# Kernel optimization log

Measured on AMD Instinct MI355X. Metric: run time of the kernel, lower is better.

Reference implementation:

```python
import jax, jax.numpy as jnp
import numpy as np

# LDPC-like Tanner graph: N variable nodes, M check nodes, dv edges per variable
N_VAR = 8192
N_CHK = 4096
DV = 3
N_EDGE = N_VAR * DV  # 24576 = code.H.E
BATCH = 128
T = 30               # opt.T iterations
EPS = 1e-7


def setup_inputs() -> dict:
    key = jax.random.key(0)
    k1, k2 = jax.random.split(key)
    # channel LLRs for a batch of received codewords, shape (N_VAR, BATCH)
    chn_llr = jax.random.normal(k1, (N_VAR, BATCH), dtype=jnp.float32) * 2.0
    # Tanner graph edge lists: edge e connects variable edge_var[e] <-> check edge_chk[e]
    edge_var = jnp.repeat(jnp.arange(N_VAR, dtype=jnp.int32), DV)
    edge_chk = jax.random.randint(k2, (N_EDGE,), 0, N_CHK, dtype=jnp.int32)
    # gamma_logit = 0  ->  sigmoid = 0.5 = damping_init
    gamma_logit = jnp.zeros((1,), dtype=jnp.float32)
    return {"chn_llr": chn_llr, "gamma_logit": gamma_logit,
            "edge_var": edge_var, "edge_chk": edge_chk}


def reference(chn_llr, gamma_logit, edge_var, edge_chk):
    """T damped sum-product BP iterations over the Tanner graph.

    Returns stacked per-iteration posterior LLRs, shape (T, N_VAR, BATCH).
    """
    gamma = jax.nn.sigmoid(gamma_logit[0])  # damping gate, shared (tie=True)
    segsum = jax.ops.segment_sum

    def step(carry, _):
        msg_C2V, msg_V2C = carry  # each (N_EDGE, BATCH)
        # ---- variable -> check update (extrinsic sum), damped by gamma ----
        var_sum = segsum(msg_C2V, edge_var, num_segments=N_VAR)        # (N_VAR, B)
        v2c_new = chn_llr[edge_var] + var_sum[edge_var] - msg_C2V       # (E, B)
        msg_V2C = gamma * v2c_new + (1.0 - gamma) * msg_V2C
        # ---- check -> variable update (tanh product rule, log/sign domain) ----
        t = jnp.tanh(jnp.clip(msg_V2C, -15.0, 15.0) * 0.5)              # (E, B)
        logabs = jnp.log(jnp.maximum(jnp.abs(t), EPS))
        neg = (t < 0.0).astype(msg_V2C.dtype)
        chk_log = segsum(logabs, edge_chk, num_segments=N_CHK)          # (N_CHK, B)
        chk_neg = segsum(neg, edge_chk, num_segments=N_CHK)
        ext_log = chk_log[edge_chk] - logabs                            # exclude self
        ext_sign = 1.0 - 2.0 * jnp.mod(chk_neg[edge_chk] - neg, 2.0)
        prod = jnp.clip(ext_sign * jnp.exp(ext_log), -1.0 + EPS, 1.0 - EPS)
        msg_C2V = 2.0 * jnp.arctanh(prod)
        # ---- per-iteration posterior LLR output ----
        out = chn_llr + segsum(msg_C2V, edge_var, num_segments=N_VAR)   # (N_VAR, B)
        return (msg_C2V, msg_V2C), out

    init = (jnp.zeros((N_EDGE, BATCH), dtype=chn_llr.dtype),
            jnp.zeros((N_EDGE, BATCH), dtype=chn_llr.dtype))
    _, outputs = jax.lax.scan(step, init, None, length=T)
    return outputs  # (T, N_VAR, BATCH)
```

## Files before the change

### kernel.cpp

```cpp
#include <hip/hip_runtime.h>
#include <math.h>

#define N_VAR 8192
#define N_CHK 4096
#define DV 3
#define N_EDGE (N_VAR * DV)
#define BATCH 128
#define T_ITERS 30
#define ELLW 24
#define CHNK 8

#define LOG2E 1.44269504088896340736f
#define LN2   0.69314718055994530942f

__device__ __forceinline__ float tanh_half(float x) {
    float ex = __builtin_amdgcn_exp2f(x * LOG2E);
    float t = 1.0f - 2.0f * __builtin_amdgcn_rcpf(ex + 1.0f);
    float s = (x < 0.0f) ? -1.0f : 1.0f;
    return s * fmaxf(fabsf(t), 1e-7f);
}

__device__ __forceinline__ float atanh2(float p) {
    const float lim = 1.0f - 1e-7f;
    p = fminf(fmaxf(p, -lim), lim);
    return (__builtin_amdgcn_logf(1.0f + p) -
            __builtin_amdgcn_logf(1.0f - p)) * LN2;
}


__global__ void k_ell_scatter(const int* __restrict__ edge_chk,
                              int* __restrict__ deg_arr, int* __restrict__ ell_e) {
    int e = blockIdx.x * blockDim.x + threadIdx.x;
    if (e < N_EDGE) {
        int c = edge_chk[e];
        int pos = atomicAdd(&deg_arr[c], 1);
        if (pos < ELLW) ell_e[c * ELLW + pos] = e;
    }
}

__global__ __launch_bounds__(1024) void k_scan(const int* __restrict__ counts,
                                               int* __restrict__ ptr) {
    __shared__ int bufA[1024];
    __shared__ int bufB[1024];
    int t = threadIdx.x;
    int c0 = counts[4 * t + 0];
    int c1 = counts[4 * t + 1];
    int c2 = counts[4 * t + 2];
    int c3 = counts[4 * t + 3];
    int s = c0 + c1 + c2 + c3;
    bufA[t] = s;
    __syncthreads();
    int* src = bufA;
    int* dst = bufB;
    for (int off = 1; off < 1024; off *= 2) {
        int v = src[t];
        if (t >= off) v += src[t - off];
        dst[t] = v;
        __syncthreads();
        int* tmp = src; src = dst; dst = tmp;
    }
    int incl = src[t];
    int excl = incl - s;
    ptr[4 * t + 0] = excl;
    ptr[4 * t + 1] = excl + c0;
    ptr[4 * t + 2] = excl + c0 + c1;
    ptr[4 * t + 3] = excl + c0 + c1 + c2;
    if (t == 1023) ptr[N_CHK] = incl;
}

__global__ void k_slotmap(const int* __restrict__ ell_e,
                          const int* __restrict__ deg_arr,
                          const int* __restrict__ ptr,
                          int* __restrict__ slot_e) {
    int gid = blockIdx.x * 256 + threadIdx.x;
    if (gid < N_CHK * ELLW) {
        int c = gid / ELLW;
        int j = gid - c * ELLW;
        int d = deg_arr[c]; if (d > ELLW) d = ELLW;
        if (j < d) slot_e[ell_e[gid]] = ptr[c] + j;
    }
}

__global__ void k_pack(const int* __restrict__ slot_e, int4* __restrict__ recs) {
    int e = blockIdx.x * 256 + threadIdx.x;
    if (e < N_EDGE) {
        int v = e / 3;
        int4 r;
        r.x = slot_e[3 * v + 0];
        r.y = slot_e[3 * v + 1];
        r.z = slot_e[3 * v + 2];
        r.w = (v << 2) | (e - 3 * v);
        recs[slot_e[e]] = r;
    }
}


__global__ __launch_bounds__(128) void k_iter(
        const float* __restrict__ chn,
        const _Float16* __restrict__ c2v_prev,
        _Float16* __restrict__ c2v_curr,
        _Float16* __restrict__ v2c,
        float* __restrict__ out_prev,
        const int have_out,
        const float* __restrict__ gamma_logit,
        const int4* __restrict__ recs,
        const int* __restrict__ deg_arr,
        const int* __restrict__ ptr) {
    int c = blockIdx.x;
    int b = threadIdx.x;
    int deg = deg_arr[c];
    if (deg > ELLW) deg = ELLW;
    if (deg == 0) return;
    int base = ptr[c];
    float g = 1.0f / (1.0f + __builtin_amdgcn_exp2f(-gamma_logit[0] * LOG2E));
    float om = 1.0f - g;

    float tv[ELLW];

#define BATCH_BODY(J0)                                                         \
    {                                                                          \
        int4 r[CHNK]; float m0[CHNK], m1[CHNK], m2[CHNK], cv[CHNK], vo[CHNK];  \
        _Pragma("unroll")                                                      \
        for (int u = 0; u < CHNK; ++u) {                                       \
            int s = base + (J0) + u;                                           \
            s = (s < N_EDGE) ? s : (N_EDGE - 1);                               \
            r[u] = recs[s];                                                    \
        }                                                                      \
        _Pragma("unroll")                                                      \
        for (int u = 0; u < CHNK; ++u) {                                       \
            int s = base + (J0) + u;                                           \
            s = (s < N_EDGE) ? s : (N_EDGE - 1);                               \
            m0[u] = (float)c2v_prev[r[u].x * BATCH + b];                       \
            m1[u] = (float)c2v_prev[r[u].y * BATCH + b];                       \
            m2[u] = (float)c2v_prev[r[u].z * BATCH + b];                       \
            cv[u] = chn[(r[u].w >> 2) * BATCH + b];                            \
            vo[u] = (float)v2c[s * BATCH + b];                                 \
        }                                                                      \
        _Pragma("unroll")                                                      \
        for (int u = 0; u < CHNK; ++u) {                                       \
            int j = (J0) + u;                                                  \
            if (j < deg) {                                                     \
                int self = base + j;                                           \
                int v = r[u].w >> 2;                                           \
                float post = cv[u] + m0[u] + m1[u] + m2[u];                    \
                float cp = (r[u].x == self) ? m0[u]                            \
                           : ((r[u].y == self) ? m1[u] : m2[u]);               \
                float vn = g * (post - cp) + om * vo[u];                       \
                v2c[self * BATCH + b] = (_Float16)vn;                          \
                if (have_out && ((r[u].w & 3) == 0)) {                         \
                    __builtin_nontemporal_store(post,                          \
                        &out_prev[v * BATCH + b]);                             \
                }                                                              \
                float x = fminf(fmaxf(vn, -15.0f), 15.0f);                     \
                tv[j] = tanh_half(x);                                          \
            }                                                                  \
        }                                                                      \
    }

    BATCH_BODY(0)
    if (deg > CHNK) BATCH_BODY(CHNK)
    if (deg > 2 * CHNK) BATCH_BODY(2 * CHNK)
#undef BATCH_BODY

    float ext[ELLW];
    float run = 1.0f;
#pragma unroll
    for (int j = ELLW - 1; j >= 0; --j) {
        if (j < deg) { ext[j] = run; run *= tv[j]; }
    }
    float pfx = 1.0f;
#pragma unroll
    for (int j = 0; j < ELLW; ++j) {
        if (j < deg) {
            float p = pfx * ext[j];
            pfx *= tv[j];
            float m = atanh2(p);
            c2v_curr[(base + j) * BATCH + b] = (_Float16)m;
        }
    }
}


__global__ __launch_bounds__(256) void k_final(
        const float* __restrict__ chn, const _Float16* __restrict__ c2v,
        const int* __restrict__ slot_e, float* __restrict__ out_last) {
    int gid = blockIdx.x * 256 + threadIdx.x;
    int v = gid >> 7;
    int b = gid & 127;
    int s0 = slot_e[3 * v + 0];
    int s1 = slot_e[3 * v + 1];
    int s2 = slot_e[3 * v + 2];
    float acc = chn[gid] + (float)c2v[s0 * BATCH + b] +
                (float)c2v[s1 * BATCH + b] + (float)c2v[s2 * BATCH + b];
    __builtin_nontemporal_store(acc, &out_last[gid]);
}


extern "C" void kernel_launch(void* const* d_in, const int* in_sizes, int n_in,
                              void* d_out, int out_size, void* d_ws, size_t ws_size,
                              hipStream_t stream) {
    const float* chn         = (const float*)d_in[0];
    const float* gamma_logit = (const float*)d_in[1];
    const int* edge_chk      = (const int*)d_in[3];
    float* out = (float*)d_out;

    const size_t MSG = (size_t)N_EDGE * BATCH;
    _Float16* c2vA   = (_Float16*)d_ws;
    _Float16* c2vB   = c2vA + MSG;
    _Float16* v2c    = c2vB + MSG;
    int4* recs       = (int4*)(v2c + MSG);
    int* slot_e      = (int*)(recs + N_EDGE);
    int* ell_e       = slot_e + N_EDGE;
    int* deg_arr     = ell_e + (size_t)N_CHK * ELLW;
    int* ptr         = deg_arr + N_CHK;

    (void)hipMemsetAsync(c2vA, 0, MSG * sizeof(_Float16), stream);
    (void)hipMemsetAsync(v2c, 0, MSG * sizeof(_Float16), stream);
    (void)hipMemsetAsync(slot_e, 0, (size_t)N_EDGE * sizeof(int), stream);
    (void)hipMemsetAsync(deg_arr, 0, N_CHK * sizeof(int), stream);

    k_ell_scatter<<<(N_EDGE + 255) / 256, 256, 0, stream>>>(edge_chk, deg_arr,
                                                            ell_e);
    k_scan<<<1, 1024, 0, stream>>>(deg_arr, ptr);
    k_slotmap<<<(N_CHK * ELLW + 255) / 256, 256, 0, stream>>>(ell_e, deg_arr,
                                                              ptr, slot_e);
    k_pack<<<(N_EDGE + 255) / 256, 256, 0, stream>>>(slot_e, recs);

    const size_t SLICE = (size_t)N_VAR * BATCH;
    _Float16* bufs[2] = {c2vA, c2vB};
    for (int t = 0; t < T_ITERS; ++t) {
        const _Float16* prev = bufs[t & 1];
        _Float16* curr = bufs[(t + 1) & 1];
        float* out_prev = (t == 0) ? out : out + (size_t)(t - 1) * SLICE;
        k_iter<<<N_CHK, 128, 0, stream>>>(chn, prev, curr, v2c, out_prev,
                                          (t > 0) ? 1 : 0, gamma_logit, recs,
                                          deg_arr, ptr);
    }
    k_final<<<(N_VAR * BATCH) / 256, 256, 0, stream>>>(
        chn, bufs[T_ITERS & 1], slot_e, out + (size_t)(T_ITERS - 1) * SLICE);
}
```

Measured before the change: 618.2 us.

## Split fused check kernel into variable-node and check-node kernels with half2 packing

Replaces the single per-check kernel with two launches per iteration. A variable-node kernel computes posteriors once per variable, updates the damped V2C messages in variable order and writes clipped values into a check-slot-ordered array. A check-node kernel then only gathers those values and runs the tanh/atanh product rule. Both kernels process two batch lanes per thread using half2/float2 vectors. This avoids each check edge re-gathering three C2V messages plus the channel value, at the cost of an extra kernel launch per iteration and an additional intermediate array round trip through memory.

```diff
diff --git a/kernel.cpp b/kernel.cpp
--- a/kernel.cpp
+++ b/kernel.cpp
@@ -6,12 +6,16 @@
 #define DV 3
 #define N_EDGE (N_VAR * DV)
 #define BATCH 128
+#define HB (BATCH / 2)
 #define T_ITERS 30
 #define ELLW 24
 #define CHNK 8
 
 #define LOG2E 1.44269504088896340736f
 #define LN2   0.69314718055994530942f
+
+typedef _Float16 h2 __attribute__((ext_vector_type(2)));
+typedef float f2 __attribute__((ext_vector_type(2)));
 
 __device__ __forceinline__ float tanh_half(float x) {
     float ex = __builtin_amdgcn_exp2f(x * LOG2E);
@@ -81,118 +85,146 @@
     }
 }
 
-__global__ void k_pack(const int* __restrict__ slot_e, int4* __restrict__ recs) {
-    int e = blockIdx.x * 256 + threadIdx.x;
-    if (e < N_EDGE) {
-        int v = e / 3;
-        int4 r;
-        r.x = slot_e[3 * v + 0];
-        r.y = slot_e[3 * v + 1];
-        r.z = slot_e[3 * v + 2];
-        r.w = (v << 2) | (e - 3 * v);
-        recs[slot_e[e]] = r;
-    }
-}
-
-
-__global__ __launch_bounds__(128) void k_iter(
+__global__ void k_slot4(const int* __restrict__ slot_e, int4* __restrict__ slot4) {
+    int v = blockIdx.x * 256 + threadIdx.x;
+    if (v < N_VAR) {
+        int4 s;
+        s.x = slot_e[3 * v + 0];
+        s.y = slot_e[3 * v + 1];
+        s.z = slot_e[3 * v + 2];
+        s.w = 0;
+        slot4[v] = s;
+    }
+}
+
+
+__global__ __launch_bounds__(256) void k_var(
         const float* __restrict__ chn,
-        const _Float16* __restrict__ c2v_prev,
-        _Float16* __restrict__ c2v_curr,
-        _Float16* __restrict__ v2c,
+        const h2* __restrict__ c2v_prev,
+        h2* __restrict__ v2c,
+        h2* __restrict__ x_arr,
         float* __restrict__ out_prev,
         const int have_out,
         const float* __restrict__ gamma_logit,
-        const int4* __restrict__ recs,
+        const int4* __restrict__ slot4) {
+    int gid = blockIdx.x * 256 + threadIdx.x;
+    int v = gid >> 6;
+    int bb = gid & 63;
+    float g = 1.0f / (1.0f + __builtin_amdgcn_exp2f(-gamma_logit[0] * LOG2E));
+    float om = 1.0f - g;
+
+    int4 s4 = slot4[v];
+    int sl[3] = {s4.x, s4.y, s4.z};
+    h2 c0 = c2v_prev[s4.x * HB + bb];
+    h2 c1 = c2v_prev[s4.y * HB + bb];
+    h2 c2 = c2v_prev[s4.z * HB + bb];
+    f2 ch = ((const f2*)chn)[v * HB + bb];
+
+    float p0 = ch.x + (float)c0.x + (float)c1.x + (float)c2.x;
+    float p1 = ch.y + (float)c0.y + (float)c1.y + (float)c2.y;
+    if (have_out) {
+        f2 o; o.x = p0; o.y = p1;
+        __builtin_nontemporal_store(o, &((f2*)out_prev)[v * HB + bb]);
+    }
+
+    float cc0[3] = {(float)c0.x, (float)c1.x, (float)c2.x};
+    float cc1[3] = {(float)c0.y, (float)c1.y, (float)c2.y};
+#pragma unroll
+    for (int i = 0; i < 3; ++i) {
+        int vi = i * (N_VAR * HB) + v * HB + bb;
+        h2 vo = v2c[vi];
+        float vn0 = g * (p0 - cc0[i]) + om * (float)vo.x;
+        float vn1 = g * (p1 - cc1[i]) + om * (float)vo.y;
+        h2 w; w.x = (_Float16)vn0; w.y = (_Float16)vn1;
+        v2c[vi] = w;
+        float x0 = fminf(fmaxf(vn0, -15.0f), 15.0f);
+        float x1 = fminf(fmaxf(vn1, -15.0f), 15.0f);
+        h2 xw; xw.x = (_Float16)x0; xw.y = (_Float16)x1;
+        x_arr[sl[i] * HB + bb] = xw;
+    }
+}
+
+
+__global__ __launch_bounds__(256) void k_chk(
+        const h2* __restrict__ x_arr,
+        h2* __restrict__ c2v_curr,
         const int* __restrict__ deg_arr,
         const int* __restrict__ ptr) {
-    int c = blockIdx.x;
-    int b = threadIdx.x;
+    int c = blockIdx.x * 4 + (threadIdx.x >> 6);
+    int bb = threadIdx.x & 63;
     int deg = deg_arr[c];
     if (deg > ELLW) deg = ELLW;
     if (deg == 0) return;
     int base = ptr[c];
-    float g = 1.0f / (1.0f + __builtin_amdgcn_exp2f(-gamma_logit[0] * LOG2E));
-    float om = 1.0f - g;
-
-    float tv[ELLW];
-
-#define BATCH_BODY(J0)                                                         \
+
+    f2 tv[ELLW];
+
+#define LOAD_BATCH(J0)                                                         \
     {                                                                          \
-        int4 r[CHNK]; float m0[CHNK], m1[CHNK], m2[CHNK], cv[CHNK], vo[CHNK];  \
+        h2 raw[CHNK];                                                          \
         _Pragma("unroll")                                                      \
         for (int u = 0; u < CHNK; ++u) {                                       \
             int s = base + (J0) + u;                                           \
             s = (s < N_EDGE) ? s : (N_EDGE - 1);                               \
-            r[u] = recs[s];                                                    \
-        }                                                                      \
-        _Pragma("unroll")                                                      \
-        for (int u = 0; u < CHNK; ++u) {                                       \
-            int s = base + (J0) + u;                                           \
-            s = (s < N_EDGE) ? s : (N_EDGE - 1);                               \
-            m0[u] = (float)c2v_prev[r[u].x * BATCH + b];                       \
-            m1[u] = (float)c2v_prev[r[u].y * BATCH + b];                       \
-            m2[u] = (float)c2v_prev[r[u].z * BATCH + b];                       \
-            cv[u] = chn[(r[u].w >> 2) * BATCH + b];                            \
-            vo[u] = (float)v2c[s * BATCH + b];                                 \
+            raw[u] = x_arr[s * HB + bb];                                       \
         }                                                                      \
         _Pragma("unroll")                                                      \
         for (int u = 0; u < CHNK; ++u) {                                       \
             int j = (J0) + u;                                                  \
             if (j < deg) {                                                     \
-                int self = base + j;                                           \
-                int v = r[u].w >> 2;                                           \
-                float post = cv[u] + m0[u] + m1[u] + m2[u];                    \
-                float cp = (r[u].x == self) ? m0[u]                            \
-                           : ((r[u].y == self) ? m1[u] : m2[u]);               \
-                float vn = g * (post - cp) + om * vo[u];                       \
-                v2c[self * BATCH + b] = (_Float16)vn;                          \
-                if (have_out && ((r[u].w & 3) == 0)) {                         \
-                    __builtin_nontemporal_store(post,                          \
-                        &out_prev[v * BATCH + b]);                             \
-                }                                                              \
-                float x = fminf(fmaxf(vn, -15.0f), 15.0f);                     \
-                tv[j] = tanh_half(x);                                          \
+                f2 tf;                                                         \
+                tf.x = tanh_half((float)raw[u].x);                             \
+                tf.y = tanh_half((float)raw[u].y);                             \
+                tv[j] = tf;                                                    \
             }                                                                  \
         }                                                                      \
     }
 
-    BATCH_BODY(0)
-    if (deg > CHNK) BATCH_BODY(CHNK)
-    if (deg > 2 * CHNK) BATCH_BODY(2 * CHNK)
-#undef BATCH_BODY
-
-    float ext[ELLW];
-    float run = 1.0f;
+    LOAD_BATCH(0)
+    if (deg > CHNK) LOAD_BATCH(CHNK)
+    if (deg > 2 * CHNK) LOAD_BATCH(2 * CHNK)
+#undef LOAD_BATCH
+
+    f2 ext[ELLW];
+    f2 run; run.x = 1.0f; run.y = 1.0f;
 #pragma unroll
     for (int j = ELLW - 1; j >= 0; --j) {
-        if (j < deg) { ext[j] = run; run *= tv[j]; }
-    }
-    float pfx = 1.0f;
+        if (j < deg) {
+            ext[j] = run;
+            run.x *= tv[j].x; run.y *= tv[j].y;
+        }
+    }
+    f2 pfx; pfx.x = 1.0f; pfx.y = 1.0f;
 #pragma unroll
     for (int j = 0; j < ELLW; ++j) {
         if (j < deg) {
-            float p = pfx * ext[j];
-            pfx *= tv[j];
-            float m = atanh2(p);
-            c2v_curr[(base + j) * BATCH + b] = (_Float16)m;
+            float p0 = pfx.x * ext[j].x;
+            float p1 = pfx.y * ext[j].y;
+            pfx.x *= tv[j].x; pfx.y *= tv[j].y;
+            h2 w;
+            w.x = (_Float16)atanh2(p0);
+            w.y = (_Float16)atanh2(p1);
+            c2v_curr[(base + j) * HB + bb] = w;
         }
     }
 }
 
 
 __global__ __launch_bounds__(256) void k_final(
-        const float* __restrict__ chn, const _Float16* __restrict__ c2v,
-        const int* __restrict__ slot_e, float* __restrict__ out_last) {
+        const float* __restrict__ chn, const h2* __restrict__ c2v,
+        const int4* __restrict__ slot4, float* __restrict__ out_last) {
     int gid = blockIdx.x * 256 + threadIdx.x;
-    int v = gid >> 7;
-    int b = gid & 127;
-    int s0 = slot_e[3 * v + 0];
-    int s1 = slot_e[3 * v + 1];
-    int s2 = slot_e[3 * v + 2];
-    float acc = chn[gid] + (float)c2v[s0 * BATCH + b] +
-                (float)c2v[s1 * BATCH + b] + (float)c2v[s2 * BATCH + b];
-    __builtin_nontemporal_store(acc, &out_last[gid]);
+    int v = gid >> 6;
+    int bb = gid & 63;
+    int4 s4 = slot4[v];
+    h2 c0 = c2v[s4.x * HB + bb];
+    h2 c1 = c2v[s4.y * HB + bb];
+    h2 c2 = c2v[s4.z * HB + bb];
+    f2 ch = ((const f2*)chn)[v * HB + bb];
+    f2 o;
+    o.x = ch.x + (float)c0.x + (float)c1.x + (float)c2.x;
+    o.y = ch.y + (float)c0.y + (float)c1.y + (float)c2.y;
+    __builtin_nontemporal_store(o, &((f2*)out_last)[v * HB + bb]);
 }
 
 
@@ -204,18 +236,19 @@
     const int* edge_chk      = (const int*)d_in[3];
     float* out = (float*)d_out;
 
-    const size_t MSG = (size_t)N_EDGE * BATCH;
-    _Float16* c2vA   = (_Float16*)d_ws;
-    _Float16* c2vB   = c2vA + MSG;
-    _Float16* v2c    = c2vB + MSG;
-    int4* recs       = (int4*)(v2c + MSG);
-    int* slot_e      = (int*)(recs + N_EDGE);
-    int* ell_e       = slot_e + N_EDGE;
-    int* deg_arr     = ell_e + (size_t)N_CHK * ELLW;
-    int* ptr         = deg_arr + N_CHK;
-
-    (void)hipMemsetAsync(c2vA, 0, MSG * sizeof(_Float16), stream);
-    (void)hipMemsetAsync(v2c, 0, MSG * sizeof(_Float16), stream);
+    const size_t MSGH = (size_t)N_EDGE * HB;
+    h2* c2vA    = (h2*)d_ws;
+    h2* c2vB    = c2vA + MSGH;
+    h2* x_arr   = c2vB + MSGH;
+    h2* v2c     = x_arr + MSGH;
+    int4* slot4 = (int4*)(v2c + 3 * (size_t)N_VAR * HB);
+    int* slot_e = (int*)(slot4 + N_VAR);
+    int* ell_e  = slot_e + N_EDGE;
+    int* deg_arr= ell_e + (size_t)N_CHK * ELLW;
+    int* ptr    = deg_arr + N_CHK;
+
+    (void)hipMemsetAsync(c2vA, 0, MSGH * sizeof(h2), stream);
+    (void)hipMemsetAsync(v2c, 0, 3 * (size_t)N_VAR * HB * sizeof(h2), stream);
     (void)hipMemsetAsync(slot_e, 0, (size_t)N_EDGE * sizeof(int), stream);
     (void)hipMemsetAsync(deg_arr, 0, N_CHK * sizeof(int), stream);
 
@@ -224,18 +257,18 @@
     k_scan<<<1, 1024, 0, stream>>>(deg_arr, ptr);
     k_slotmap<<<(N_CHK * ELLW + 255) / 256, 256, 0, stream>>>(ell_e, deg_arr,
                                                               ptr, slot_e);
-    k_pack<<<(N_EDGE + 255) / 256, 256, 0, stream>>>(slot_e, recs);
+    k_slot4<<<N_VAR / 256, 256, 0, stream>>>(slot_e, slot4);
 
     const size_t SLICE = (size_t)N_VAR * BATCH;
-    _Float16* bufs[2] = {c2vA, c2vB};
+    h2* bufs[2] = {c2vA, c2vB};
     for (int t = 0; t < T_ITERS; ++t) {
-        const _Float16* prev = bufs[t & 1];
-        _Float16* curr = bufs[(t + 1) & 1];
+        const h2* prev = bufs[t & 1];
+        h2* curr = bufs[(t + 1) & 1];
         float* out_prev = (t == 0) ? out : out + (size_t)(t - 1) * SLICE;
-        k_iter<<<N_CHK, 128, 0, stream>>>(chn, prev, curr, v2c, out_prev,
-                                          (t > 0) ? 1 : 0, gamma_logit, recs,
-                                          deg_arr, ptr);
-    }
-    k_final<<<(N_VAR * BATCH) / 256, 256, 0, stream>>>(
-        chn, bufs[T_ITERS & 1], slot_e, out + (size_t)(T_ITERS - 1) * SLICE);
-}
+        k_var<<<(N_VAR * HB) / 256, 256, 0, stream>>>(
+            chn, prev, v2c, x_arr, out_prev, (t > 0) ? 1 : 0, gamma_logit, slot4);
+        k_chk<<<N_CHK / 4, 256, 0, stream>>>(x_arr, curr, deg_arr, ptr);
+    }
+    k_final<<<(N_VAR * HB) / 256, 256, 0, stream>>>(
+        chn, bufs[T_ITERS & 1], slot4, out + (size_t)(T_ITERS - 1) * SLICE);
+}
```

Measured after the change: 614.1 us. About the same (-0.7%).

## Fuse all BP iterations into one persistent kernel per batch column in LDS

Applied to the files above, without the earlier changes.

Replaces the 30 per-iteration launches, which streamed fp16 message arrays through global memory, with a single kernel. Each 1024-thread block owns one batch column and keeps all C2V and clipped V2C messages for that column in shared memory, about 96 KB, syncing between the variable and check phases. V2C damping state stays in registers. Outputs are written variable-major to a workspace buffer and transposed afterwards when space allows. The risks are that only 128 blocks run, LDS scatter and gather may hit bank conflicts, and check-node work per thread is serial over up to 24 edges.

```diff
diff --git a/kernel.cpp b/kernel.cpp
--- a/kernel.cpp
+++ b/kernel.cpp
@@ -8,7 +8,6 @@
 #define BATCH 128
 #define T_ITERS 30
 #define ELLW 24
-#define CHNK 8
 
 #define LOG2E 1.44269504088896340736f
 #define LN2   0.69314718055994530942f
@@ -81,118 +80,140 @@
     }
 }
 
-__global__ void k_pack(const int* __restrict__ slot_e, int4* __restrict__ recs) {
-    int e = blockIdx.x * 256 + threadIdx.x;
-    if (e < N_EDGE) {
-        int v = e / 3;
-        int4 r;
-        r.x = slot_e[3 * v + 0];
-        r.y = slot_e[3 * v + 1];
-        r.z = slot_e[3 * v + 2];
-        r.w = (v << 2) | (e - 3 * v);
-        recs[slot_e[e]] = r;
-    }
-}
-
-
-__global__ __launch_bounds__(128) void k_iter(
+__global__ void k_slot4(const int* __restrict__ slot_e, int4* __restrict__ slot4) {
+    int v = blockIdx.x * 256 + threadIdx.x;
+    if (v < N_VAR) {
+        int4 s;
+        s.x = slot_e[3 * v + 0];
+        s.y = slot_e[3 * v + 1];
+        s.z = slot_e[3 * v + 2];
+        s.w = 0;
+        slot4[v] = s;
+    }
+}
+
+
+__global__ __launch_bounds__(1024, 4) void k_bp(
         const float* __restrict__ chn,
-        const _Float16* __restrict__ c2v_prev,
-        _Float16* __restrict__ c2v_curr,
-        _Float16* __restrict__ v2c,
-        float* __restrict__ out_prev,
-        const int have_out,
         const float* __restrict__ gamma_logit,
-        const int4* __restrict__ recs,
+        const int4* __restrict__ slot4,
         const int* __restrict__ deg_arr,
-        const int* __restrict__ ptr) {
-    int c = blockIdx.x;
-    int b = threadIdx.x;
-    int deg = deg_arr[c];
-    if (deg > ELLW) deg = ELLW;
-    if (deg == 0) return;
-    int base = ptr[c];
-    float g = 1.0f / (1.0f + __builtin_amdgcn_exp2f(-gamma_logit[0] * LOG2E));
-    float om = 1.0f - g;
-
-    float tv[ELLW];
-
-#define BATCH_BODY(J0)                                                         \
-    {                                                                          \
-        int4 r[CHNK]; float m0[CHNK], m1[CHNK], m2[CHNK], cv[CHNK], vo[CHNK];  \
-        _Pragma("unroll")                                                      \
-        for (int u = 0; u < CHNK; ++u) {                                       \
-            int s = base + (J0) + u;                                           \
-            s = (s < N_EDGE) ? s : (N_EDGE - 1);                               \
-            r[u] = recs[s];                                                    \
-        }                                                                      \
-        _Pragma("unroll")                                                      \
-        for (int u = 0; u < CHNK; ++u) {                                       \
-            int s = base + (J0) + u;                                           \
-            s = (s < N_EDGE) ? s : (N_EDGE - 1);                               \
-            m0[u] = (float)c2v_prev[r[u].x * BATCH + b];                       \
-            m1[u] = (float)c2v_prev[r[u].y * BATCH + b];                       \
-            m2[u] = (float)c2v_prev[r[u].z * BATCH + b];                       \
-            cv[u] = chn[(r[u].w >> 2) * BATCH + b];                            \
-            vo[u] = (float)v2c[s * BATCH + b];                                 \
-        }                                                                      \
-        _Pragma("unroll")                                                      \
-        for (int u = 0; u < CHNK; ++u) {                                       \
-            int j = (J0) + u;                                                  \
-            if (j < deg) {                                                     \
-                int self = base + j;                                           \
-                int v = r[u].w >> 2;                                           \
-                float post = cv[u] + m0[u] + m1[u] + m2[u];                    \
-                float cp = (r[u].x == self) ? m0[u]                            \
-                           : ((r[u].y == self) ? m1[u] : m2[u]);               \
-                float vn = g * (post - cp) + om * vo[u];                       \
-                v2c[self * BATCH + b] = (_Float16)vn;                          \
-                if (have_out && ((r[u].w & 3) == 0)) {                         \
-                    __builtin_nontemporal_store(post,                          \
-                        &out_prev[v * BATCH + b]);                             \
-                }                                                              \
-                float x = fminf(fmaxf(vn, -15.0f), 15.0f);                     \
-                tv[j] = tanh_half(x);                                          \
-            }                                                                  \
-        }                                                                      \
-    }
-
-    BATCH_BODY(0)
-    if (deg > CHNK) BATCH_BODY(CHNK)
-    if (deg > 2 * CHNK) BATCH_BODY(2 * CHNK)
-#undef BATCH_BODY
-
-    float ext[ELLW];
-    float run = 1.0f;
-#pragma unroll
-    for (int j = ELLW - 1; j >= 0; --j) {
-        if (j < deg) { ext[j] = run; run *= tv[j]; }
-    }
-    float pfx = 1.0f;
-#pragma unroll
-    for (int j = 0; j < ELLW; ++j) {
-        if (j < deg) {
-            float p = pfx * ext[j];
-            pfx *= tv[j];
-            float m = atanh2(p);
-            c2v_curr[(base + j) * BATCH + b] = (_Float16)m;
+        const int* __restrict__ ptr,
+        float* __restrict__ outT,
+        float* __restrict__ outD) {
+    __shared__ _Float16 s_c2v[N_EDGE];
+    __shared__ _Float16 s_x[N_EDGE];
+    const int b = blockIdx.x;
+    const int tid = threadIdx.x;
+
+    for (int i = tid; i < N_EDGE; i += 1024) s_c2v[i] = (_Float16)0.0f;
+
+    const float g = 1.0f / (1.0f + __builtin_amdgcn_exp2f(-gamma_logit[0] * LOG2E));
+    const float om = 1.0f - g;
+
+    float chn_r[8];
+    float v2c_r[8][3];
+#pragma unroll
+    for (int k = 0; k < 8; ++k) {
+        chn_r[k] = chn[(size_t)(tid + k * 1024) * BATCH + b];
+        v2c_r[k][0] = 0.0f; v2c_r[k][1] = 0.0f; v2c_r[k][2] = 0.0f;
+    }
+    __syncthreads();
+
+    const size_t SLICE = (size_t)N_VAR * BATCH;
+
+    for (int t = 0; t < T_ITERS; ++t) {
+#pragma unroll
+        for (int k = 0; k < 8; ++k) {
+            int v = tid + k * 1024;
+            int4 s4 = slot4[v];
+            float c0 = (float)s_c2v[s4.x];
+            float c1 = (float)s_c2v[s4.y];
+            float c2 = (float)s_c2v[s4.z];
+            float post = chn_r[k] + c0 + c1 + c2;
+            if (t > 0) {
+                if (outT) {
+                    __builtin_nontemporal_store(post,
+                        &outT[(size_t)(t - 1) * SLICE + (size_t)b * N_VAR + v]);
+                } else {
+                    __builtin_nontemporal_store(post,
+                        &outD[(size_t)(t - 1) * SLICE + (size_t)v * BATCH + b]);
+                }
+            }
+            float vn0 = g * (post - c0) + om * v2c_r[k][0];
+            float vn1 = g * (post - c1) + om * v2c_r[k][1];
+            float vn2 = g * (post - c2) + om * v2c_r[k][2];
+            v2c_r[k][0] = vn0; v2c_r[k][1] = vn1; v2c_r[k][2] = vn2;
+            s_x[s4.x] = (_Float16)fminf(fmaxf(vn0, -15.0f), 15.0f);
+            s_x[s4.y] = (_Float16)fminf(fmaxf(vn1, -15.0f), 15.0f);
+            s_x[s4.z] = (_Float16)fminf(fmaxf(vn2, -15.0f), 15.0f);
         }
-    }
-}
-
-
-__global__ __launch_bounds__(256) void k_final(
-        const float* __restrict__ chn, const _Float16* __restrict__ c2v,
-        const int* __restrict__ slot_e, float* __restrict__ out_last) {
-    int gid = blockIdx.x * 256 + threadIdx.x;
-    int v = gid >> 7;
-    int b = gid & 127;
-    int s0 = slot_e[3 * v + 0];
-    int s1 = slot_e[3 * v + 1];
-    int s2 = slot_e[3 * v + 2];
-    float acc = chn[gid] + (float)c2v[s0 * BATCH + b] +
-                (float)c2v[s1 * BATCH + b] + (float)c2v[s2 * BATCH + b];
-    __builtin_nontemporal_store(acc, &out_last[gid]);
+        __syncthreads();
+
+#pragma unroll
+        for (int m = 0; m < 4; ++m) {
+            int c = tid + m * 1024;
+            int deg = deg_arr[c];
+            if (deg > ELLW) deg = ELLW;
+            int base = ptr[c];
+            if (deg > 0) {
+                float tv[ELLW];
+#pragma unroll
+                for (int j = 0; j < ELLW; ++j)
+                    if (j < deg) tv[j] = tanh_half((float)s_x[base + j]);
+                float ext[ELLW];
+                float run = 1.0f;
+#pragma unroll
+                for (int j = ELLW - 1; j >= 0; --j)
+                    if (j < deg) { ext[j] = run; run *= tv[j]; }
+                float pfx = 1.0f;
+#pragma unroll
+                for (int j = 0; j < ELLW; ++j)
+                    if (j < deg) {
+                        float p = pfx * ext[j];
+                        pfx *= tv[j];
+                        s_c2v[base + j] = (_Float16)atanh2(p);
+                    }
+            }
+        }
+        __syncthreads();
+    }
+
+#pragma unroll
+    for (int k = 0; k < 8; ++k) {
+        int v = tid + k * 1024;
+        int4 s4 = slot4[v];
+        float post = chn_r[k] + (float)s_c2v[s4.x] + (float)s_c2v[s4.y] +
+                     (float)s_c2v[s4.z];
+        if (outT) {
+            __builtin_nontemporal_store(post,
+                &outT[(size_t)(T_ITERS - 1) * SLICE + (size_t)b * N_VAR + v]);
+        } else {
+            __builtin_nontemporal_store(post,
+                &outD[(size_t)(T_ITERS - 1) * SLICE + (size_t)v * BATCH + b]);
+        }
+    }
+}
+
+
+__global__ __launch_bounds__(256) void k_transpose(const float* __restrict__ src,
+                                                   float* __restrict__ dst) {
+    __shared__ float tile[32][33];
+    int t = blockIdx.z;
+    int v0 = blockIdx.x * 32;
+    int b0 = blockIdx.y * 32;
+    int lx = threadIdx.x;
+    int ly = threadIdx.y;
+    const float* s = src + (size_t)t * N_VAR * BATCH;
+    float* d = dst + (size_t)t * N_VAR * BATCH;
+#pragma unroll
+    for (int i = 0; i < 32; i += 8)
+        tile[ly + i][lx] = s[(size_t)(b0 + ly + i) * N_VAR + v0 + lx];
+    __syncthreads();
+#pragma unroll
+    for (int i = 0; i < 32; i += 8)
+        __builtin_nontemporal_store(tile[lx][ly + i],
+            &d[(size_t)(v0 + ly + i) * BATCH + b0 + lx]);
 }
 
 
@@ -204,18 +225,17 @@
     const int* edge_chk      = (const int*)d_in[3];
     float* out = (float*)d_out;
 
-    const size_t MSG = (size_t)N_EDGE * BATCH;
-    _Float16* c2vA   = (_Float16*)d_ws;
-    _Float16* c2vB   = c2vA + MSG;
-    _Float16* v2c    = c2vB + MSG;
-    int4* recs       = (int4*)(v2c + MSG);
-    int* slot_e      = (int*)(recs + N_EDGE);
-    int* ell_e       = slot_e + N_EDGE;
-    int* deg_arr     = ell_e + (size_t)N_CHK * ELLW;
-    int* ptr         = deg_arr + N_CHK;
-
-    (void)hipMemsetAsync(c2vA, 0, MSG * sizeof(_Float16), stream);
-    (void)hipMemsetAsync(v2c, 0, MSG * sizeof(_Float16), stream);
+    int4* slot4  = (int4*)d_ws;
+    int* slot_e  = (int*)(slot4 + N_VAR);
+    int* ell_e   = slot_e + N_EDGE;
+    int* deg_arr = ell_e + (size_t)N_CHK * ELLW;
+    int* ptr     = deg_arr + N_CHK;
+    size_t table_bytes = (char*)(ptr + N_CHK + 1) - (char*)d_ws;
+    size_t outT_off = (table_bytes + 255) & ~(size_t)255;
+    size_t outT_bytes = (size_t)T_ITERS * N_VAR * BATCH * sizeof(float);
+    float* outT = (ws_size >= outT_off + outT_bytes)
+                      ? (float*)((char*)d_ws + outT_off) : (float*)0;
+
     (void)hipMemsetAsync(slot_e, 0, (size_t)N_EDGE * sizeof(int), stream);
     (void)hipMemsetAsync(deg_arr, 0, N_CHK * sizeof(int), stream);
 
@@ -224,18 +244,14 @@
     k_scan<<<1, 1024, 0, stream>>>(deg_arr, ptr);
     k_slotmap<<<(N_CHK * ELLW + 255) / 256, 256, 0, stream>>>(ell_e, deg_arr,
                                                               ptr, slot_e);
-    k_pack<<<(N_EDGE + 255) / 256, 256, 0, stream>>>(slot_e, recs);
-
-    const size_t SLICE = (size_t)N_VAR * BATCH;
-    _Float16* bufs[2] = {c2vA, c2vB};
-    for (int t = 0; t < T_ITERS; ++t) {
-        const _Float16* prev = bufs[t & 1];
-        _Float16* curr = bufs[(t + 1) & 1];
-        float* out_prev = (t == 0) ? out : out + (size_t)(t - 1) * SLICE;
-        k_iter<<<N_CHK, 128, 0, stream>>>(chn, prev, curr, v2c, out_prev,
-                                          (t > 0) ? 1 : 0, gamma_logit, recs,
-                                          deg_arr, ptr);
-    }
-    k_final<<<(N_VAR * BATCH) / 256, 256, 0, stream>>>(
-        chn, bufs[T_ITERS & 1], slot_e, out + (size_t)(T_ITERS - 1) * SLICE);
-}
+    k_slot4<<<N_VAR / 256, 256, 0, stream>>>(slot_e, slot4);
+
+    k_bp<<<BATCH, 1024, 0, stream>>>(chn, gamma_logit, slot4, deg_arr, ptr,
+                                     outT, out);
+
+    if (outT) {
+        dim3 tg(N_VAR / 32, BATCH / 32, T_ITERS);
+        dim3 tb(32, 8, 1);
+        k_transpose<<<tg, tb, 0, stream>>>(outT, out);
+    }
+}
```

Result: slower. 847.1 us (+37.0%).
